# Performance work log

Hardware: AMD Instinct MI355X
Metric: run time of the kernel (lower is better)

Reference implementation:

```python
import jax, jax.numpy as jnp
import numpy as np

H, D, V, B, M = 1024, 512, 50257, 256, 100000


def setup_inputs() -> dict:
    key = jax.random.key(0)
    ks = jax.random.split(key, 16)
    s = 0.02
    return {
        "hidden_state": jax.random.normal(ks[0], (B, H), jnp.float32),
        "memory_keys": jax.random.normal(ks[1], (M, D), jnp.float32),
        "memory_values": jax.random.normal(ks[2], (M, D), jnp.float32),
        "importance": jax.random.uniform(ks[3], (M,), jnp.float32),
        "Wq": jax.random.normal(ks[4], (D, H), jnp.float32) * s,
        "bq": jnp.zeros((D,), jnp.float32),
        "Wp1": jax.random.normal(ks[5], (H, H + D), jnp.float32) * s,
        "bp1": jnp.zeros((H,), jnp.float32),
        "Wp2": jax.random.normal(ks[6], (V, H), jnp.float32) * s,
        "bp2": jnp.zeros((V,), jnp.float32),
        "Wv1": jax.random.normal(ks[7], (H, H + D), jnp.float32) * s,
        "bv1": jnp.zeros((H,), jnp.float32),
        "Wv2": jax.random.normal(ks[8], (1, H), jnp.float32) * s,
        "bv2": jnp.zeros((1,), jnp.float32),
        "top_k": 8,
    }


def reference(hidden_state, memory_keys, memory_values, importance,
              Wq, bq, Wp1, bp1, Wp2, bp2, Wv1, bv1, Wv2, bv2, top_k):
    # --- query generation (query_generator Linear) ---
    query = hidden_state @ Wq.T + bq  # [B, D]
    # --- content-addressable retrieval: cosine similarity x importance weight ---
    qn = query / (jnp.linalg.norm(query, axis=-1, keepdims=True) + 1e-8)
    kn = memory_keys / (jnp.linalg.norm(memory_keys, axis=-1, keepdims=True) + 1e-8)
    sims = (qn @ kn.T) * importance[None, :]  # [B, M]
    top_s, top_i = jax.lax.top_k(sims, top_k)  # [B, K]
    attn = jax.nn.softmax(top_s, axis=-1)  # [B, K]
    gathered = memory_values[top_i]  # [B, K, D] gather from memory bank
    memory_context = jnp.einsum("bk,bkd->bd", attn, gathered)  # [B, D]
    # --- PPO PolicyNetwork: policy head + value head on concat(hidden, context) ---
    combined = jnp.concatenate([hidden_state, memory_context], axis=-1)  # [B, H+D]
    h_p = jax.nn.relu(combined @ Wp1.T + bp1)
    logits = h_p @ Wp2.T + bp2  # [B, V]
    h_v = jax.nn.relu(combined @ Wv1.T + bv1)
    value = h_v @ Wv2.T + bv2  # [B, 1]
    return logits, value
```

## Files before the change

kernel.cpp:

```cpp
#include <hip/hip_runtime.h>
#include <math.h>
#include <stdint.h>
#include <stddef.h>

#define BB 256
#define HHDIM 1024
#define DDIM 512
#define VDIM 50257
#define MMEM 100000

typedef __attribute__((ext_vector_type(8))) short bf8_t;
typedef __attribute__((ext_vector_type(4))) float f4_t;
typedef __attribute__((ext_vector_type(4))) unsigned short us4_t;

static __device__ __forceinline__ unsigned short f2bf(float x) {
    union { float f; uint32_t u; } a; a.f = x;
    uint32_t r = a.u + 0x7FFFu + ((a.u >> 16) & 1u);
    return (unsigned short)(r >> 16);
}
static __device__ __forceinline__ float bf2f(unsigned short s) {
    union { uint32_t u; float f; } a; a.u = ((uint32_t)s) << 16; return a.f;
}

template<int BM, int BN>
__global__ __launch_bounds__(256) void gemm_f32_kernel(
    const float* __restrict__ A1, int K1, const float* __restrict__ A2, int K2,
    const float* __restrict__ Wa, const float* __restrict__ ba,
    const float* __restrict__ Wb, const float* __restrict__ bbias,
    int NSPLIT, int N, int RELU, float* __restrict__ C,
    unsigned short* __restrict__ ghout)
{
    const int K = K1 + K2;
    const int RM = BM / 16, RN = BN / 16;
    __shared__ float As[BM][33];
    __shared__ float Ws[BN][33];
    int t = threadIdx.x;
    int tx = t & 15, ty = t >> 4;
    int bb0 = blockIdx.x * BM;
    int nb0 = blockIdx.y * BN;
    float c[RM][RN];
#pragma unroll
    for (int i = 0; i < RM; ++i)
#pragma unroll
        for (int j = 0; j < RN; ++j) c[i][j] = 0.f;

    for (int k0 = 0; k0 < K; k0 += 32) {
        for (int idx = t; idx < BM * 8; idx += 256) {
            int row = idx >> 3, kq = idx & 7;
            int gk = k0 + kq * 4;
            float4 v;
            if (gk < K1) v = *(const float4*)(A1 + (size_t)(bb0 + row) * K1 + gk);
            else         v = *(const float4*)(A2 + (size_t)(bb0 + row) * K2 + (gk - K1));
            As[row][kq * 4 + 0] = v.x; As[row][kq * 4 + 1] = v.y;
            As[row][kq * 4 + 2] = v.z; As[row][kq * 4 + 3] = v.w;
        }
        for (int idx = t; idx < BN * 8; idx += 256) {
            int row = idx >> 3, kq = idx & 7;
            int gk = k0 + kq * 4;
            int n = nb0 + row;
            const float* wr = (n < NSPLIT) ? (Wa + (size_t)n * K)
                                           : (Wb + (size_t)(n - NSPLIT) * K);
            float4 v = *(const float4*)(wr + gk);
            Ws[row][kq * 4 + 0] = v.x; Ws[row][kq * 4 + 1] = v.y;
            Ws[row][kq * 4 + 2] = v.z; Ws[row][kq * 4 + 3] = v.w;
        }
        __syncthreads();
#pragma unroll
        for (int k = 0; k < 32; ++k) {
            float a[RM], w[RN];
#pragma unroll
            for (int i = 0; i < RM; ++i) a[i] = As[ty * RM + i][k];
#pragma unroll
            for (int j = 0; j < RN; ++j) w[j] = Ws[tx * RN + j][k];
#pragma unroll
            for (int i = 0; i < RM; ++i)
#pragma unroll
                for (int j = 0; j < RN; ++j) c[i][j] = fmaf(a[i], w[j], c[i][j]);
        }
        __syncthreads();
    }
#pragma unroll
    for (int i = 0; i < RM; ++i) {
#pragma unroll
        for (int j = 0; j < RN; ++j) {
            int b = bb0 + ty * RM + i;
            int n = nb0 + tx * RN + j;
            float bias = (n < NSPLIT) ? ba[n] : bbias[n - NSPLIT];
            float v = c[i][j] + bias;
            if (RELU) v = fmaxf(v, 0.f);
            C[(size_t)b * N + n] = v;
            if (ghout != nullptr && n < NSPLIT)
                ghout[(size_t)b * NSPLIT + n] = f2bf(v);
        }
    }
}

__global__ __launch_bounds__(256) void qprep_kernel(
    const float* __restrict__ query, float* __restrict__ qinv,
    unsigned short* __restrict__ gq)
{
    int b = blockIdx.x, t = threadIdx.x;
    int lane = t & 63, wid = t >> 6;
    __shared__ float red[4];
    float x0 = query[(size_t)b * 512 + t];
    float x1 = query[(size_t)b * 512 + 256 + t];
    float ss = x0 * x0 + x1 * x1;
#pragma unroll
    for (int off = 32; off; off >>= 1) ss += __shfl_down(ss, off);
    if (lane == 0) red[wid] = ss;
    __syncthreads();
    if (t == 0) qinv[b] = 1.0f / (sqrtf(red[0] + red[1] + red[2] + red[3]) + 1e-8f);
    gq[(size_t)b * 512 + t] = f2bf(x0);
    gq[(size_t)b * 512 + 256 + t] = f2bf(x1);
}

__global__ __launch_bounds__(256, 2) void sims_kernel(
    const float* __restrict__ keys, const float* __restrict__ imp,
    const unsigned short* __restrict__ gq, const float* __restrict__ qinv,
    unsigned short* __restrict__ scores)
{
    __shared__ unsigned short Aq[256 * 32];
    __shared__ unsigned short Bk[128 * 32];
    __shared__ float sumsq_s[128];
    __shared__ float scale_s[128];
    __shared__ float qinv_s[256];
    int t = threadIdx.x, lane = t & 63, wid = t >> 6;
    int fr = lane & 15, fq = lane >> 4;
    int mbase = blockIdx.x * 128;
    int b0 = (wid >> 1) * 128;
    int m0 = (wid & 1) * 64;
    qinv_s[t] = qinv[t];
    if (t < 128) sumsq_s[t] = 0.f;

    f4_t acc[8][4];
#pragma unroll
    for (int i = 0; i < 8; ++i)
#pragma unroll
        for (int j = 0; j < 4; ++j) acc[i][j] = (f4_t){0.f, 0.f, 0.f, 0.f};
    float ps[4] = {0.f, 0.f, 0.f, 0.f};

    const int arow0 = t >> 2, ach = t & 3;
    const int bml0 = t >> 3, bkq = t & 7;

    for (int step = 0; step < 16; ++step) {
#pragma unroll
        for (int j = 0; j < 4; ++j) {
            int row = arow0 + 64 * j;
            bf8_t v = *(const bf8_t*)(const void*)(gq + (size_t)row * 512 + step * 32 + ach * 8);
            int slot = ach ^ ((row >> 1) & 3);
            *(bf8_t*)(void*)(&Aq[row * 32 + slot * 8]) = v;
        }
#pragma unroll
        for (int jj = 0; jj < 4; ++jj) {
            int ml = bml0 + 32 * jj;
            int gm = mbase + ml;
            float4 v = {0.f, 0.f, 0.f, 0.f};
            if (gm < MMEM) v = *(const float4*)(keys + (size_t)gm * 512 + step * 32 + bkq * 4);
            ps[jj] += v.x * v.x + v.y * v.y + v.z * v.z + v.w * v.w;
            us4_t pk; pk[0] = f2bf(v.x); pk[1] = f2bf(v.y); pk[2] = f2bf(v.z); pk[3] = f2bf(v.w);
            int slot = (bkq >> 1) ^ ((ml >> 1) & 3);
            *(us4_t*)(void*)(&Bk[ml * 32 + slot * 8 + (bkq & 1) * 4]) = pk;
        }
        __syncthreads();
        bf8_t af[8], bfr[4];
        int slotr = fq ^ ((fr >> 1) & 3);
#pragma unroll
        for (int i = 0; i < 8; ++i)
            af[i] = *(const bf8_t*)(const void*)(&Aq[(b0 + i * 16 + fr) * 32 + slotr * 8]);
#pragma unroll
        for (int j = 0; j < 4; ++j)
            bfr[j] = *(const bf8_t*)(const void*)(&Bk[(m0 + j * 16 + fr) * 32 + slotr * 8]);
#pragma unroll
        for (int i = 0; i < 8; ++i)
#pragma unroll
            for (int j = 0; j < 4; ++j)
                acc[i][j] = __builtin_amdgcn_mfma_f32_16x16x32_bf16(af[i], bfr[j], acc[i][j], 0, 0, 0);
        __syncthreads();
    }
#pragma unroll
    for (int jj = 0; jj < 4; ++jj) atomicAdd(&sumsq_s[bml0 + 32 * jj], ps[jj]);
    __syncthreads();
    if (t < 128) {
        int gm = mbase + t;
        float im = (gm < MMEM) ? imp[gm] : 0.f;
        scale_s[t] = im / (sqrtf(sumsq_s[t]) + 1e-8f);
    }
    __syncthreads();
#pragma unroll
    for (int i = 0; i < 8; ++i) {
        int brow = b0 + i * 16 + fq * 4;
#pragma unroll
        for (int j = 0; j < 4; ++j) {
            int mloc = m0 + j * 16 + fr;
            int gm = mbase + mloc;
            if (gm < MMEM) {
                float sc = scale_s[mloc];
#pragma unroll
                for (int r = 0; r < 4; ++r) {
                    float val = acc[i][j][r] * sc * qinv_s[brow + r];
                    scores[(size_t)(brow + r) * MMEM + gm] = f2bf(val);
                }
            }
        }
    }
}

#define TK_CHUNK 4096
#define TK_NCH   25

__global__ __launch_bounds__(256) void topk_stage1_kernel(
    const unsigned short* __restrict__ scores,
    float* __restrict__ cand_val, int* __restrict__ cand_idx)
{
    int chunk = blockIdx.x, b = blockIdx.y;
    int t = threadIdx.x, lane = t & 63, wid = t >> 6;
    __shared__ float wval[4]; __shared__ int wpay[4];
    __shared__ int winner_s;
    const unsigned short* srow = scores + (size_t)b * MMEM;
    int base = chunk * TK_CHUNK;
    int m0 = base + t * 16;
    float v[16];
    if (m0 + 16 <= MMEM) {
        bf8_t s0 = *(const bf8_t*)(const void*)(srow + m0);
        bf8_t s1 = *(const bf8_t*)(const void*)(srow + m0 + 8);
#pragma unroll
        for (int j = 0; j < 8; ++j) v[j] = bf2f((unsigned short)s0[j]);
#pragma unroll
        for (int j = 0; j < 8; ++j) v[8 + j] = bf2f((unsigned short)s1[j]);
    } else {
#pragma unroll
        for (int j = 0; j < 16; ++j)
            v[j] = (m0 + j < MMEM) ? bf2f(srow[m0 + j]) : -1e30f;
    }
    float bm = v[0]; int bp = 0;
#pragma unroll
    for (int p = 1; p < 16; ++p) if (v[p] > bm) { bm = v[p]; bp = p; }

    for (int r = 0; r < 16; ++r) {
        float mv = bm; int mp = (t << 4) | bp;
#pragma unroll
        for (int off = 32; off; off >>= 1) {
            float ov = __shfl_down(mv, off); int op = __shfl_down(mp, off);
            if (ov > mv) { mv = ov; mp = op; }
        }
        if (lane == 0) { wval[wid] = mv; wpay[wid] = mp; }
        __syncthreads();
        if (t == 0) {
            float bv = wval[0]; int bpay = wpay[0];
#pragma unroll
            for (int w = 1; w < 4; ++w) if (wval[w] > bv) { bv = wval[w]; bpay = wpay[w]; }
            int o = ((b * TK_NCH + chunk) << 4) | r;
            cand_val[o] = bv;
            cand_idx[o] = base + (bpay >> 4) * 16 + (bpay & 15);
            winner_s = bpay;
        }
        __syncthreads();
        if (t == (winner_s >> 4)) {
            int slot = winner_s & 15;
#pragma unroll
            for (int p = 0; p < 16; ++p) if (p == slot) v[p] = -1e30f;
            bm = v[0]; bp = 0;
#pragma unroll
            for (int p = 1; p < 16; ++p) if (v[p] > bm) { bm = v[p]; bp = p; }
        }
    }
}

__global__ __launch_bounds__(256) void topk_refine2_kernel(
    const float* __restrict__ cand_val, const int* __restrict__ cand_idx,
    const float* __restrict__ keys, const float* __restrict__ values,
    const float* __restrict__ imp, const float* __restrict__ query,
    const float* __restrict__ qinv, float* __restrict__ context)
{
    int b = blockIdx.x, t = threadIdx.x;
    int lane = t & 63, wid = t >> 6;
    __shared__ float q_s[512];
    __shared__ float wval[4]; __shared__ int wpay[4];
    __shared__ int winner_s;
    __shared__ int cidx[16]; __shared__ float csc[16];
    __shared__ float attn_s[8]; __shared__ int vidx_s[8];

    q_s[t] = query[(size_t)b * 512 + t];
    q_s[t + 256] = query[(size_t)b * 512 + 256 + t];

    const float* cvb = cand_val + b * (TK_NCH * 16);
    const int*   cib = cand_idx + b * (TK_NCH * 16);
    float v0 = cvb[t]; int i0 = cib[t];
    float v1 = -1e30f;  int i1 = 0;
    if (t < TK_NCH * 16 - 256) { v1 = cvb[t + 256]; i1 = cib[t + 256]; }
    float bm; int bp;
    if (v1 > v0) { bm = v1; bp = 1; } else { bm = v0; bp = 0; }

    for (int r = 0; r < 16; ++r) {
        float mv = bm; int mp = (t << 1) | bp;
#pragma unroll
        for (int off = 32; off; off >>= 1) {
            float ov = __shfl_down(mv, off); int op = __shfl_down(mp, off);
            if (ov > mv) { mv = ov; mp = op; }
        }
        if (lane == 0) { wval[wid] = mv; wpay[wid] = mp; }
        __syncthreads();
        if (t == 0) {
            float bv = wval[0]; int bpay = wpay[0];
#pragma unroll
            for (int w = 1; w < 4; ++w) if (wval[w] > bv) { bv = wval[w]; bpay = wpay[w]; }
            winner_s = bpay;
        }
        __syncthreads();
        if (t == (winner_s >> 1)) {
            int slot = winner_s & 1;
            cidx[r] = slot ? i1 : i0;
            if (slot == 0) v0 = -1e30f; else v1 = -1e30f;
            if (v1 > v0) { bm = v1; bp = 1; } else { bm = v0; bp = 0; }
        }
    }
    __syncthreads();
    for (int cc = 0; cc < 4; ++cc) {
        int c = wid * 4 + cc;
        int mi = cidx[c];
        const float* krow = keys + (size_t)mi * 512;
        float4 k1 = *(const float4*)(krow + lane * 8);
        float4 k2 = *(const float4*)(krow + lane * 8 + 4);
        int q0 = lane * 8;
        float dot = k1.x * q_s[q0] + k1.y * q_s[q0 + 1] + k1.z * q_s[q0 + 2] + k1.w * q_s[q0 + 3]
                  + k2.x * q_s[q0 + 4] + k2.y * q_s[q0 + 5] + k2.z * q_s[q0 + 6] + k2.w * q_s[q0 + 7];
        float nr = k1.x * k1.x + k1.y * k1.y + k1.z * k1.z + k1.w * k1.w
                 + k2.x * k2.x + k2.y * k2.y + k2.z * k2.z + k2.w * k2.w;
#pragma unroll
        for (int off = 32; off; off >>= 1) {
            dot += __shfl_down(dot, off);
            nr  += __shfl_down(nr, off);
        }
        if (lane == 0)
            csc[c] = dot * qinv[b] * imp[mi] / (sqrtf(nr) + 1e-8f);
    }
    __syncthreads();
    if (t == 0) {
        unsigned used = 0;
        float sv[8]; int si[8];
#pragma unroll
        for (int r = 0; r < 8; ++r) {
            float bmx = -1e31f; int bpp = 0;
            for (int p = 0; p < 16; ++p)
                if (!((used >> p) & 1u) && csc[p] > bmx) { bmx = csc[p]; bpp = p; }
            used |= 1u << bpp; sv[r] = bmx; si[r] = cidx[bpp];
        }
        float mx = sv[0];
        float ee[8]; float den = 0.f;
#pragma unroll
        for (int r = 0; r < 8; ++r) { ee[r] = expf(sv[r] - mx); den += ee[r]; }
#pragma unroll
        for (int r = 0; r < 8; ++r) { attn_s[r] = ee[r] / den; vidx_s[r] = si[r]; }
    }
    __syncthreads();
    int d0 = t * 2;
    float c0 = 0.f, c1 = 0.f;
#pragma unroll
    for (int r = 0; r < 8; ++r) {
        float w = attn_s[r];
        const float* vrow = values + (size_t)vidx_s[r] * 512;
        float2 vv = *(const float2*)(vrow + d0);
        c0 += w * vv.x; c1 += w * vv.y;
    }
    float2 outv; outv.x = c0; outv.y = c1;
    *(float2*)(context + (size_t)b * 512 + d0) = outv;
}

__global__ __launch_bounds__(256, 2) void logits_kernel(
    const float* __restrict__ Wp2, const float* __restrict__ bp2,
    const unsigned short* __restrict__ gh, float* __restrict__ out)
{
    __shared__ unsigned short Ah[256 * 32];
    __shared__ unsigned short Bw[128 * 32];
    __shared__ float bias_s[128];
    int t = threadIdx.x, lane = t & 63, wid = t >> 6;
    int fr = lane & 15, fq = lane >> 4;
    int vbase = blockIdx.x * 128;
    int b0 = (wid >> 1) * 128;
    int m0 = (wid & 1) * 64;
    if (t < 128) { int gv = vbase + t; bias_s[t] = (gv < VDIM) ? bp2[gv] : 0.f; }

    f4_t acc[8][4];
#pragma unroll
    for (int i = 0; i < 8; ++i)
#pragma unroll
        for (int j = 0; j < 4; ++j) acc[i][j] = (f4_t){0.f, 0.f, 0.f, 0.f};

    const int arow0 = t >> 2, ach = t & 3;
    const int bml0 = t >> 3, bkq = t & 7;

    for (int step = 0; step < 32; ++step) {
#pragma unroll
        for (int j = 0; j < 4; ++j) {
            int row = arow0 + 64 * j;
            bf8_t v = *(const bf8_t*)(const void*)(gh + (size_t)row * 1024 + step * 32 + ach * 8);
            int slot = ach ^ ((row >> 1) & 3);
            *(bf8_t*)(void*)(&Ah[row * 32 + slot * 8]) = v;
        }
#pragma unroll
        for (int jj = 0; jj < 4; ++jj) {
            int ml = bml0 + 32 * jj;
            int gv = vbase + ml;
            float4 v = {0.f, 0.f, 0.f, 0.f};
            if (gv < VDIM) v = *(const float4*)(Wp2 + (size_t)gv * 1024 + step * 32 + bkq * 4);
            us4_t pk; pk[0] = f2bf(v.x); pk[1] = f2bf(v.y); pk[2] = f2bf(v.z); pk[3] = f2bf(v.w);
            int slot = (bkq >> 1) ^ ((ml >> 1) & 3);
            *(us4_t*)(void*)(&Bw[ml * 32 + slot * 8 + (bkq & 1) * 4]) = pk;
        }
        __syncthreads();
        bf8_t af[8], bfr[4];
        int slotr = fq ^ ((fr >> 1) & 3);
#pragma unroll
        for (int i = 0; i < 8; ++i)
            af[i] = *(const bf8_t*)(const void*)(&Ah[(b0 + i * 16 + fr) * 32 + slotr * 8]);
#pragma unroll
        for (int j = 0; j < 4; ++j)
            bfr[j] = *(const bf8_t*)(const void*)(&Bw[(m0 + j * 16 + fr) * 32 + slotr * 8]);
#pragma unroll
        for (int i = 0; i < 8; ++i)
#pragma unroll
            for (int j = 0; j < 4; ++j)
                acc[i][j] = __builtin_amdgcn_mfma_f32_16x16x32_bf16(af[i], bfr[j], acc[i][j], 0, 0, 0);
        __syncthreads();
    }
#pragma unroll
    for (int i = 0; i < 8; ++i) {
        int brow = b0 + i * 16 + fq * 4;
#pragma unroll
        for (int j = 0; j < 4; ++j) {
            int vloc = m0 + j * 16 + fr;
            int gv = vbase + vloc;
            if (gv < VDIM) {
                float bias = bias_s[vloc];
#pragma unroll
                for (int r = 0; r < 4; ++r)
                    out[(size_t)(brow + r) * VDIM + gv] = acc[i][j][r] + bias;
            }
        }
    }
}

__global__ __launch_bounds__(256) void value_kernel(
    const float* __restrict__ hcomb, const float* __restrict__ Wv2,
    const float* __restrict__ bv2, float* __restrict__ out)
{
    int lane = threadIdx.x & 63, wid = threadIdx.x >> 6;
    int b = blockIdx.x * 4 + wid;
    float s = 0.f;
#pragma unroll
    for (int i = 0; i < 16; ++i) {
        int k = lane + 64 * i;
        s += hcomb[(size_t)b * 2048 + 1024 + k] * Wv2[k];
    }
#pragma unroll
    for (int off = 32; off; off >>= 1) s += __shfl_down(s, off);
    if (lane == 0) out[(size_t)BB * VDIM + b] = s + bv2[0];
}

extern "C" void kernel_launch(void* const* d_in, const int* in_sizes, int n_in,
                              void* d_out, int out_size, void* d_ws, size_t ws_size,
                              hipStream_t stream)
{
    const float* hidden = (const float*)d_in[0];
    const float* keys   = (const float*)d_in[1];
    const float* values = (const float*)d_in[2];
    const float* imp    = (const float*)d_in[3];
    const float* Wq  = (const float*)d_in[4];
    const float* bq  = (const float*)d_in[5];
    const float* Wp1 = (const float*)d_in[6];
    const float* bp1 = (const float*)d_in[7];
    const float* Wp2 = (const float*)d_in[8];
    const float* bp2 = (const float*)d_in[9];
    const float* Wv1 = (const float*)d_in[10];
    const float* bv1 = (const float*)d_in[11];
    const float* Wv2 = (const float*)d_in[12];
    const float* bv2 = (const float*)d_in[13];
    float* out = (float*)d_out;
    char* ws = (char*)d_ws;

    float*          query   = (float*)(ws + 0);
    float*          qinv    = (float*)(ws + 524288);
    unsigned short* gq      = (unsigned short*)(ws + 525312);
    float*          context = (float*)(ws + 787456);
    float*          hcomb   = (float*)(ws + 1311744);
    unsigned short* gh      = (unsigned short*)(ws + 3408896);
    unsigned short* scores  = (unsigned short*)(ws + 3933184);
    float* cand_val = (float*)(ws + 1311744);
    int*   cand_idx = (int*)  (ws + 1311744 + 409600);

    gemm_f32_kernel<16, 64><<<dim3(16, 8), 256, 0, stream>>>(
        hidden, 1024, nullptr, 0, Wq, bq, nullptr, nullptr, 512, 512, 0, query, nullptr);
    qprep_kernel<<<256, 256, 0, stream>>>(query, qinv, gq);
    sims_kernel<<<782, 256, 0, stream>>>(keys, imp, gq, qinv, scores);
    topk_stage1_kernel<<<dim3(TK_NCH, 256), 256, 0, stream>>>(scores, cand_val, cand_idx);
    topk_refine2_kernel<<<256, 256, 0, stream>>>(
        cand_val, cand_idx, keys, values, imp, query, qinv, context);
    gemm_f32_kernel<32, 64><<<dim3(8, 32), 256, 0, stream>>>(
        hidden, 1024, context, 512, Wp1, bp1, Wv1, bv1, 1024, 2048, 1, hcomb, gh);
    logits_kernel<<<393, 256, 0, stream>>>(Wp2, bp2, gh, out);
    value_kernel<<<64, 256, 0, stream>>>(hcomb, Wv2, bv2, out);
}
```

Before: 1.016 ms.

## Double-buffer LDS tiles with direct global-to-LDS loads in sims and logits GEMMs

Both the sims and logits bf16 MFMA kernels now use two LDS buffers. The next K-step's fp32 weight/key tiles are prefetched into registers and the bf16 activation tile is loaded straight into LDS with global_load_lds, while MFMAs run on the current buffer. The goal is to hide global-load latency and drop one barrier per step. LDS use per block doubles, which may cut occupancy under launch_bounds(256,2). The A-tile swizzle is moved from the LDS write side to the global read addresses.

```diff
diff --git a/kernel.cpp b/kernel.cpp
--- a/kernel.cpp
+++ b/kernel.cpp
@@ -20,6 +20,12 @@
 }
 static __device__ __forceinline__ float bf2f(unsigned short s) {
     union { uint32_t u; float f; } a; a.u = ((uint32_t)s) << 16; return a.f;
+}
+
+static __device__ __forceinline__ void glds16(const unsigned short* g, unsigned short* l) {
+    __builtin_amdgcn_global_load_lds(
+        (const __attribute__((address_space(1))) unsigned int*)g,
+        (__attribute__((address_space(3))) unsigned int*)l, 16, 0, 0);
 }
 
 template<int BM, int BN>
@@ -119,8 +125,8 @@
     const unsigned short* __restrict__ gq, const float* __restrict__ qinv,
     unsigned short* __restrict__ scores)
 {
-    __shared__ unsigned short Aq[256 * 32];
-    __shared__ unsigned short Bk[128 * 32];
+    __shared__ unsigned short Aq[2][256 * 32];
+    __shared__ unsigned short Bk[2][128 * 32];
     __shared__ float sumsq_s[128];
     __shared__ float scale_s[128];
     __shared__ float qinv_s[256];
@@ -139,42 +145,77 @@
         for (int j = 0; j < 4; ++j) acc[i][j] = (f4_t){0.f, 0.f, 0.f, 0.f};
     float ps[4] = {0.f, 0.f, 0.f, 0.f};
 
-    const int arow0 = t >> 2, ach = t & 3;
     const int bml0 = t >> 3, bkq = t & 7;
-
-    for (int step = 0; step < 16; ++step) {
-#pragma unroll
-        for (int j = 0; j < 4; ++j) {
-            int row = arow0 + 64 * j;
-            bf8_t v = *(const bf8_t*)(const void*)(gq + (size_t)row * 512 + step * 32 + ach * 8);
-            int slot = ach ^ ((row >> 1) & 3);
-            *(bf8_t*)(void*)(&Aq[row * 32 + slot * 8]) = v;
-        }
-#pragma unroll
-        for (int jj = 0; jj < 4; ++jj) {
-            int ml = bml0 + 32 * jj;
-            int gm = mbase + ml;
-            float4 v = {0.f, 0.f, 0.f, 0.f};
-            if (gm < MMEM) v = *(const float4*)(keys + (size_t)gm * 512 + step * 32 + bkq * 4);
-            ps[jj] += v.x * v.x + v.y * v.y + v.z * v.z + v.w * v.w;
-            us4_t pk; pk[0] = f2bf(v.x); pk[1] = f2bf(v.y); pk[2] = f2bf(v.z); pk[3] = f2bf(v.w);
-            int slot = (bkq >> 1) ^ ((ml >> 1) & 3);
-            *(us4_t*)(void*)(&Bk[ml * 32 + slot * 8 + (bkq & 1) * 4]) = pk;
-        }
-        __syncthreads();
+    int   gmr[4];  bool gmv[4];
+#pragma unroll
+    for (int jj = 0; jj < 4; ++jj) {
+        gmr[jj] = mbase + bml0 + 32 * jj;
+        gmv[jj] = gmr[jj] < MMEM;
+    }
+
+#pragma unroll
+    for (int j = 0; j < 4; ++j) {
+        int c = t + 256 * j;
+        int row = c >> 2, slot = c & 3;
+        int ach = slot ^ ((row >> 1) & 3);
+        glds16(gq + (size_t)row * 512 + ach * 8, &Aq[0][c * 8]);
+    }
+    float4 kreg[4];
+#pragma unroll
+    for (int jj = 0; jj < 4; ++jj)
+        kreg[jj] = gmv[jj] ? *(const float4*)(keys + (size_t)gmr[jj] * 512 + bkq * 4)
+                           : (float4){0.f, 0.f, 0.f, 0.f};
+#pragma unroll
+    for (int jj = 0; jj < 4; ++jj) {
+        int ml = bml0 + 32 * jj;
+        float4 v = kreg[jj];
+        ps[jj] += v.x * v.x + v.y * v.y + v.z * v.z + v.w * v.w;
+        us4_t pk; pk[0] = f2bf(v.x); pk[1] = f2bf(v.y); pk[2] = f2bf(v.z); pk[3] = f2bf(v.w);
+        int slot = (bkq >> 1) ^ ((ml >> 1) & 3);
+        *(us4_t*)(void*)(&Bk[0][ml * 32 + slot * 8 + (bkq & 1) * 4]) = pk;
+    }
+    __syncthreads();
+
+    for (int s = 0; s < 16; ++s) {
+        int cur = s & 1, nxt = cur ^ 1;
+        if (s < 15) {
+#pragma unroll
+            for (int jj = 0; jj < 4; ++jj)
+                kreg[jj] = gmv[jj]
+                    ? *(const float4*)(keys + (size_t)gmr[jj] * 512 + (s + 1) * 32 + bkq * 4)
+                    : (float4){0.f, 0.f, 0.f, 0.f};
+#pragma unroll
+            for (int j = 0; j < 4; ++j) {
+                int c = t + 256 * j;
+                int row = c >> 2, slot = c & 3;
+                int ach = slot ^ ((row >> 1) & 3);
+                glds16(gq + (size_t)row * 512 + (s + 1) * 32 + ach * 8, &Aq[nxt][c * 8]);
+            }
+        }
         bf8_t af[8], bfr[4];
         int slotr = fq ^ ((fr >> 1) & 3);
 #pragma unroll
         for (int i = 0; i < 8; ++i)
-            af[i] = *(const bf8_t*)(const void*)(&Aq[(b0 + i * 16 + fr) * 32 + slotr * 8]);
+            af[i] = *(const bf8_t*)(const void*)(&Aq[cur][(b0 + i * 16 + fr) * 32 + slotr * 8]);
 #pragma unroll
         for (int j = 0; j < 4; ++j)
-            bfr[j] = *(const bf8_t*)(const void*)(&Bk[(m0 + j * 16 + fr) * 32 + slotr * 8]);
+            bfr[j] = *(const bf8_t*)(const void*)(&Bk[cur][(m0 + j * 16 + fr) * 32 + slotr * 8]);
 #pragma unroll
         for (int i = 0; i < 8; ++i)
 #pragma unroll
             for (int j = 0; j < 4; ++j)
                 acc[i][j] = __builtin_amdgcn_mfma_f32_16x16x32_bf16(af[i], bfr[j], acc[i][j], 0, 0, 0);
+        if (s < 15) {
+#pragma unroll
+            for (int jj = 0; jj < 4; ++jj) {
+                int ml = bml0 + 32 * jj;
+                float4 v = kreg[jj];
+                ps[jj] += v.x * v.x + v.y * v.y + v.z * v.z + v.w * v.w;
+                us4_t pk; pk[0] = f2bf(v.x); pk[1] = f2bf(v.y); pk[2] = f2bf(v.z); pk[3] = f2bf(v.w);
+                int slot = (bkq >> 1) ^ ((ml >> 1) & 3);
+                *(us4_t*)(void*)(&Bk[nxt][ml * 32 + slot * 8 + (bkq & 1) * 4]) = pk;
+            }
+        }
         __syncthreads();
     }
 #pragma unroll
@@ -370,8 +411,8 @@
     const float* __restrict__ Wp2, const float* __restrict__ bp2,
     const unsigned short* __restrict__ gh, float* __restrict__ out)
 {
-    __shared__ unsigned short Ah[256 * 32];
-    __shared__ unsigned short Bw[128 * 32];
+    __shared__ unsigned short Ah[2][256 * 32];
+    __shared__ unsigned short Bw[2][128 * 32];
     __shared__ float bias_s[128];
     int t = threadIdx.x, lane = t & 63, wid = t >> 6;
     int fr = lane & 15, fq = lane >> 4;
@@ -386,41 +427,75 @@
 #pragma unroll
         for (int j = 0; j < 4; ++j) acc[i][j] = (f4_t){0.f, 0.f, 0.f, 0.f};
 
-    const int arow0 = t >> 2, ach = t & 3;
     const int bml0 = t >> 3, bkq = t & 7;
-
-    for (int step = 0; step < 32; ++step) {
-#pragma unroll
-        for (int j = 0; j < 4; ++j) {
-            int row = arow0 + 64 * j;
-            bf8_t v = *(const bf8_t*)(const void*)(gh + (size_t)row * 1024 + step * 32 + ach * 8);
-            int slot = ach ^ ((row >> 1) & 3);
-            *(bf8_t*)(void*)(&Ah[row * 32 + slot * 8]) = v;
-        }
-#pragma unroll
-        for (int jj = 0; jj < 4; ++jj) {
-            int ml = bml0 + 32 * jj;
-            int gv = vbase + ml;
-            float4 v = {0.f, 0.f, 0.f, 0.f};
-            if (gv < VDIM) v = *(const float4*)(Wp2 + (size_t)gv * 1024 + step * 32 + bkq * 4);
-            us4_t pk; pk[0] = f2bf(v.x); pk[1] = f2bf(v.y); pk[2] = f2bf(v.z); pk[3] = f2bf(v.w);
-            int slot = (bkq >> 1) ^ ((ml >> 1) & 3);
-            *(us4_t*)(void*)(&Bw[ml * 32 + slot * 8 + (bkq & 1) * 4]) = pk;
-        }
-        __syncthreads();
+    int   gvr[4];  bool gvv[4];
+#pragma unroll
+    for (int jj = 0; jj < 4; ++jj) {
+        gvr[jj] = vbase + bml0 + 32 * jj;
+        gvv[jj] = gvr[jj] < VDIM;
+    }
+
+#pragma unroll
+    for (int j = 0; j < 4; ++j) {
+        int c = t + 256 * j;
+        int row = c >> 2, slot = c & 3;
+        int ach = slot ^ ((row >> 1) & 3);
+        glds16(gh + (size_t)row * 1024 + ach * 8, &Ah[0][c * 8]);
+    }
+    float4 kreg[4];
+#pragma unroll
+    for (int jj = 0; jj < 4; ++jj)
+        kreg[jj] = gvv[jj] ? *(const float4*)(Wp2 + (size_t)gvr[jj] * 1024 + bkq * 4)
+                           : (float4){0.f, 0.f, 0.f, 0.f};
+#pragma unroll
+    for (int jj = 0; jj < 4; ++jj) {
+        int ml = bml0 + 32 * jj;
+        float4 v = kreg[jj];
+        us4_t pk; pk[0] = f2bf(v.x); pk[1] = f2bf(v.y); pk[2] = f2bf(v.z); pk[3] = f2bf(v.w);
+        int slot = (bkq >> 1) ^ ((ml >> 1) & 3);
+        *(us4_t*)(void*)(&Bw[0][ml * 32 + slot * 8 + (bkq & 1) * 4]) = pk;
+    }
+    __syncthreads();
+
+    for (int s = 0; s < 32; ++s) {
+        int cur = s & 1, nxt = cur ^ 1;
+        if (s < 31) {
+#pragma unroll
+            for (int jj = 0; jj < 4; ++jj)
+                kreg[jj] = gvv[jj]
+                    ? *(const float4*)(Wp2 + (size_t)gvr[jj] * 1024 + (s + 1) * 32 + bkq * 4)
+                    : (float4){0.f, 0.f, 0.f, 0.f};
+#pragma unroll
+            for (int j = 0; j < 4; ++j) {
+                int c = t + 256 * j;
+                int row = c >> 2, slot = c & 3;
+                int ach = slot ^ ((row >> 1) & 3);
+                glds16(gh + (size_t)row * 1024 + (s + 1) * 32 + ach * 8, &Ah[nxt][c * 8]);
+            }
+        }
         bf8_t af[8], bfr[4];
         int slotr = fq ^ ((fr >> 1) & 3);
 #pragma unroll
         for (int i = 0; i < 8; ++i)
-            af[i] = *(const bf8_t*)(const void*)(&Ah[(b0 + i * 16 + fr) * 32 + slotr * 8]);
+            af[i] = *(const bf8_t*)(const void*)(&Ah[cur][(b0 + i * 16 + fr) * 32 + slotr * 8]);
 #pragma unroll
         for (int j = 0; j < 4; ++j)
-            bfr[j] = *(const bf8_t*)(const void*)(&Bw[(m0 + j * 16 + fr) * 32 + slotr * 8]);
+            bfr[j] = *(const bf8_t*)(const void*)(&Bw[cur][(m0 + j * 16 + fr) * 32 + slotr * 8]);
 #pragma unroll
         for (int i = 0; i < 8; ++i)
 #pragma unroll
             for (int j = 0; j < 4; ++j)
                 acc[i][j] = __builtin_amdgcn_mfma_f32_16x16x32_bf16(af[i], bfr[j], acc[i][j], 0, 0, 0);
+        if (s < 31) {
+#pragma unroll
+            for (int jj = 0; jj < 4; ++jj) {
+                int ml = bml0 + 32 * jj;
+                float4 v = kreg[jj];
+                us4_t pk; pk[0] = f2bf(v.x); pk[1] = f2bf(v.y); pk[2] = f2bf(v.z); pk[3] = f2bf(v.w);
+                int slot = (bkq >> 1) ^ ((ml >> 1) & 3);
+                *(us4_t*)(void*)(&Bw[nxt][ml * 32 + slot * 8 + (bkq & 1) * 4]) = pk;
+            }
+        }
         __syncthreads();
     }
 #pragma unroll
```

New measurement: 910.0 us. 10.5% less time.
